# Kernel tuning notes

Hardware: AMD Instinct MI355X
Metric: run time of the kernel (lower is better)

Reference implementation:

```python
import jax, jax.numpy as jnp
import numpy as np

N = 50000
E = 600000
C = 128
O = 128


def setup_inputs() -> dict:
    key = jax.random.key(0)
    ks = jax.random.split(key, 10)
    return {
        "x": jax.random.normal(ks[0], (N, C), dtype=jnp.float32),
        "edge_weight": jax.random.uniform(ks[1], (E,), dtype=jnp.float32),
        "w0": jax.random.normal(ks[2], (C, O), dtype=jnp.float32) / np.sqrt(C),
        "b0": jax.random.normal(ks[3], (O,), dtype=jnp.float32) * 0.01,
        "w1": jax.random.normal(ks[4], (C, O), dtype=jnp.float32) / np.sqrt(C),
        "b1": jax.random.normal(ks[5], (O,), dtype=jnp.float32) * 0.01,
        "w2": jax.random.normal(ks[6], (C, O), dtype=jnp.float32) / np.sqrt(C),
        "b2": jax.random.normal(ks[7], (O,), dtype=jnp.float32) * 0.01,
        "row": jax.random.randint(ks[8], (E,), 0, N, dtype=jnp.int64),
        "col": jax.random.randint(ks[9], (E,), 0, N, dtype=jnp.int64),
    }


def reference(x, edge_weight, w0, b0, w1, b1, w2, b2, row, col):
    n = x.shape[0]

    def spmm(v):
        # out[i] = sum_{e: row[e]==i} edge_weight[e] * v[col[e]]
        return jax.ops.segment_sum(edge_weight[:, None] * v[col], row, num_segments=n)

    x0 = x @ w0 + b0                    # hop 0: no propagation
    x1 = spmm(x @ w1 + b1)              # hop 1: one SpMM
    x2 = spmm(spmm(x @ w2 + b2))        # hop 2: two SpMMs
    return jnp.concatenate([x0, x1, x2], axis=1)  # [N, 3*O]
```

## Files before the change

### kernel.cpp

```cpp
#include <hip/hip_runtime.h>
#include <hip/hip_bf16.h>


#define NC 128
#define BM 64
#define BK 32
#define SBLK 256


__global__ void zero_kernel(int* __restrict__ p, int n) {
    int i = blockIdx.x * blockDim.x + threadIdx.x;
    if (i < n) p[i] = 0;
}


__global__ void count_kernel(const int* __restrict__ row, const float* __restrict__ ew,
                             int* __restrict__ cnt, float* __restrict__ s1, int E) {
    int e = blockIdx.x * blockDim.x + threadIdx.x;
    if (e < E) {
        int r = row[e];
        atomicAdd(&cnt[r], 1);
        atomicAdd(&s1[r], ew[e]);
    }
}

__global__ __launch_bounds__(SBLK) void scan_partial(const int* __restrict__ cnt,
                                                     int* __restrict__ bsum, int n) {
    int i = blockIdx.x * SBLK + threadIdx.x;
    int v = (i < n) ? cnt[i] : 0;
    #pragma unroll
    for (int off = 32; off; off >>= 1) v += __shfl_down(v, off, 64);
    __shared__ int wsum[4];
    if ((threadIdx.x & 63) == 0) wsum[threadIdx.x >> 6] = v;
    __syncthreads();
    if (threadIdx.x == 0) bsum[blockIdx.x] = wsum[0] + wsum[1] + wsum[2] + wsum[3];
}

__global__ __launch_bounds__(SBLK) void scan_base(const int* __restrict__ bsum,
                                                  int* __restrict__ bbase, int nb) {
    __shared__ int sh[SBLK];
    int tid = threadIdx.x;
    int v = (tid < nb) ? bsum[tid] : 0;
    sh[tid] = v;
    __syncthreads();
    for (int off = 1; off < SBLK; off <<= 1) {
        int add = (tid >= off) ? sh[tid - off] : 0;
        __syncthreads();
        sh[tid] += add;
        __syncthreads();
    }
    if (tid < nb) bbase[tid] = sh[tid] - v;
}

__global__ __launch_bounds__(SBLK) void scan_final(const int* __restrict__ cnt,
                                                   const int* __restrict__ bbase,
                                                   int* __restrict__ rowptr,
                                                   int* __restrict__ pos, int n, int E) {
    int i = blockIdx.x * SBLK + threadIdx.x;
    int tid = threadIdx.x;
    __shared__ int sh[SBLK];
    int v = (i < n) ? cnt[i] : 0;
    sh[tid] = v;
    __syncthreads();
    for (int off = 1; off < SBLK; off <<= 1) {
        int add = (tid >= off) ? sh[tid - off] : 0;
        __syncthreads();
        sh[tid] += add;
        __syncthreads();
    }
    int excl = sh[tid] - v + bbase[blockIdx.x];
    if (i < n) { rowptr[i] = excl; pos[i] = excl; }
    if (i == 0) rowptr[n] = E;
}

__global__ void scatter_kernel(const int* __restrict__ row, const int* __restrict__ col,
                               const float* __restrict__ ew, int* __restrict__ pos,
                               int* __restrict__ ccol, float* __restrict__ cw, int E) {
    int e = blockIdx.x * blockDim.x + threadIdx.x;
    if (e < E) {
        int r = row[e];
        int p = atomicAdd(&pos[r], 1);
        if (p >= 0 && p < E) {
            ccol[p] = col[e];
            cw[p]   = ew[e];
        }
    }
}

__global__ void s2_kernel(const int* __restrict__ rowptr, const int* __restrict__ ccol,
                          const float* __restrict__ cw, const float* __restrict__ s1,
                          float* __restrict__ s2, int n) {
    int i = blockIdx.x * blockDim.x + threadIdx.x;
    if (i >= n) return;
    int s = rowptr[i], e = rowptr[i + 1];
    float acc = 0.f;
    for (int k = s; k < e; k++) acc += cw[k] * s1[ccol[k]];
    s2[i] = acc;
}


__global__ __launch_bounds__(256) void spmm_kernel(
    const int* __restrict__ rowptr, const int* __restrict__ ccol,
    const float* __restrict__ cw, const float* __restrict__ v,
    float* __restrict__ out, int n)
{
    int wid = (blockIdx.x * blockDim.x + threadIdx.x) >> 6;
    int lane = threadIdx.x & 63;
    if (wid >= n) return;
    int s = rowptr[wid];
    int e = rowptr[wid + 1];
    float ax = 0.f, ay = 0.f;
    int k = s;
    for (; k + 4 <= e; k += 4) {
        int c0 = ccol[k], c1 = ccol[k + 1], c2 = ccol[k + 2], c3 = ccol[k + 3];
        float w0 = cw[k], w1 = cw[k + 1], w2 = cw[k + 2], w3 = cw[k + 3];
        float2 v0 = *(const float2*)(v + (size_t)c0 * NC + lane * 2);
        float2 v1 = *(const float2*)(v + (size_t)c1 * NC + lane * 2);
        float2 v2 = *(const float2*)(v + (size_t)c2 * NC + lane * 2);
        float2 v3 = *(const float2*)(v + (size_t)c3 * NC + lane * 2);
        ax += w0 * v0.x; ay += w0 * v0.y;
        ax += w1 * v1.x; ay += w1 * v1.y;
        ax += w2 * v2.x; ay += w2 * v2.y;
        ax += w3 * v3.x; ay += w3 * v3.y;
    }
    for (; k < e; k++) {
        int c = ccol[k];
        float w = cw[k];
        float2 vv = *(const float2*)(v + (size_t)c * NC + lane * 2);
        ax += w * vv.x; ay += w * vv.y;
    }
    float2* o = (float2*)(out + (size_t)wid * NC + lane * 2);
    *o = {ax, ay};
}


__global__ __launch_bounds__(256, 4) void gemm3_kernel(
    const float* __restrict__ x, const float* __restrict__ Y1, const float* __restrict__ Y2,
    const float* __restrict__ w0, const float* __restrict__ b0,
    const float* __restrict__ w1, const float* __restrict__ b1,
    const float* __restrict__ w2, const float* __restrict__ b2,
    const float* __restrict__ s1, const float* __restrict__ s2,
    float* __restrict__ out, int n)
{
    __shared__ float xs[BK][BM];
    __shared__ float wsb[BK][NC];

    int hop = blockIdx.y;
    const float* S  = (hop == 0) ? x  : (hop == 1) ? Y1 : Y2;
    const float* W  = (hop == 0) ? w0 : (hop == 1) ? w1 : w2;
    const float* B  = (hop == 0) ? b0 : (hop == 1) ? b1 : b2;
    const float* SV = (hop == 0) ? nullptr : (hop == 1) ? s1 : s2;

    int tid = threadIdx.x;
    int m0 = blockIdx.x * BM;
    int tx = tid & 31, ty = tid >> 5;
    int c0 = tx * 4, r0 = ty * 8;

    int sr = tid >> 2;
    int skk = (tid & 3) * 8;
    int gr_s = m0 + sr;
    bool inb = (gr_s < n);

    float acc[8][4] = {};

    for (int kc = 0; kc < NC; kc += BK) {
        if (kc) __syncthreads();
        float4 a0 = {0,0,0,0}, a1 = {0,0,0,0};
        if (inb) {
            const float4* xv = (const float4*)(S + (size_t)gr_s * NC + kc + skk);
            a0 = xv[0]; a1 = xv[1];
        }
        xs[skk + 0][sr] = a0.x; xs[skk + 1][sr] = a0.y;
        xs[skk + 2][sr] = a0.z; xs[skk + 3][sr] = a0.w;
        xs[skk + 4][sr] = a1.x; xs[skk + 5][sr] = a1.y;
        xs[skk + 6][sr] = a1.z; xs[skk + 7][sr] = a1.w;
        {
            const float4* Wv = (const float4*)(W + (size_t)kc * NC);
            float4* wv = (float4*)&wsb[0][0];
            wv[tid]       = Wv[tid];
            wv[tid + 256] = Wv[tid + 256];
            wv[tid + 512] = Wv[tid + 512];
            wv[tid + 768] = Wv[tid + 768];
        }
        __syncthreads();

        #pragma unroll 8
        for (int k = 0; k < BK; k++) {
            float4 bv = *(const float4*)&wsb[k][c0];
            float4 x0 = *(const float4*)&xs[k][r0];
            float4 x1 = *(const float4*)&xs[k][r0 + 4];
            float a[8] = {x0.x, x0.y, x0.z, x0.w, x1.x, x1.y, x1.z, x1.w};
            #pragma unroll
            for (int i = 0; i < 8; i++) {
                acc[i][0] += a[i] * bv.x;
                acc[i][1] += a[i] * bv.y;
                acc[i][2] += a[i] * bv.z;
                acc[i][3] += a[i] * bv.w;
            }
        }
    }

    float4 bb = *(const float4*)(B + c0);
    #pragma unroll
    for (int i = 0; i < 8; i++) {
        int gr = m0 + r0 + i;
        if (gr < n) {
            float sc = SV ? SV[gr] : 1.0f;
            float4 v = {acc[i][0] + sc * bb.x, acc[i][1] + sc * bb.y,
                        acc[i][2] + sc * bb.z, acc[i][3] + sc * bb.w};
            *(float4*)(out + (size_t)gr * 384 + hop * NC + c0) = v;
        }
    }
}


extern "C" void kernel_launch(void* const* d_in, const int* in_sizes, int n_in,
                              void* d_out, int out_size, void* d_ws, size_t ws_size,
                              hipStream_t stream) {
    const float* x  = (const float*)d_in[0];
    const float* ew = (const float*)d_in[1];
    const float* w0 = (const float*)d_in[2];
    const float* b0 = (const float*)d_in[3];
    const float* w1 = (const float*)d_in[4];
    const float* b1 = (const float*)d_in[5];
    const float* w2 = (const float*)d_in[6];
    const float* b2 = (const float*)d_in[7];
    const int* row  = (const int*)d_in[8];
    const int* col  = (const int*)d_in[9];
    float* out = (float*)d_out;

    const int N = in_sizes[0] / NC;
    const int E = in_sizes[1];

    char* ws = (char*)d_ws;
    size_t off = 0;
    auto alloc = [&](size_t bytes) {
        void* p = ws + off;
        off += (bytes + 255) & ~(size_t)255;
        return p;
    };
    float* Y1    = (float*)alloc((size_t)N * NC * 4);
    float* Y2    = (float*)alloc((size_t)N * NC * 4);
    int* cnt     = (int*)alloc((size_t)2 * N * 4);
    float* s1    = (float*)(cnt + N);
    int* rowptr  = (int*)alloc((size_t)(N + 1) * 4);
    int* pos     = (int*)alloc((size_t)N * 4);
    float* s2    = (float*)alloc((size_t)N * 4);
    int* ccol    = (int*)alloc((size_t)E * 4);
    float* cw    = (float*)alloc((size_t)E * 4);

    int nb = (N + SBLK - 1) / SBLK;
    int* bsum  = (int*)alloc((size_t)nb * 4);
    int* bbase = (int*)alloc((size_t)nb * 4);

    zero_kernel<<<(2 * N + 255) / 256, 256, 0, stream>>>(cnt, 2 * N);
    count_kernel<<<(E + 255) / 256, 256, 0, stream>>>(row, ew, cnt, s1, E);
    scan_partial<<<nb, SBLK, 0, stream>>>(cnt, bsum, N);
    scan_base<<<1, SBLK, 0, stream>>>(bsum, bbase, nb);
    scan_final<<<nb, SBLK, 0, stream>>>(cnt, bbase, rowptr, pos, N, E);
    scatter_kernel<<<(E + 255) / 256, 256, 0, stream>>>(row, col, ew, pos, ccol, cw, E);
    s2_kernel<<<(N + 255) / 256, 256, 0, stream>>>(rowptr, ccol, cw, s1, s2, N);

    int spmm_blocks = (N * 64 + 255) / 256;
    spmm_kernel<<<spmm_blocks, 256, 0, stream>>>(rowptr, ccol, cw, x, Y1, N);
    spmm_kernel<<<spmm_blocks, 256, 0, stream>>>(rowptr, ccol, cw, Y1, Y2, N);

    gemm3_kernel<<<dim3((N + BM - 1) / BM, 3), 256, 0, stream>>>(
        x, Y1, Y2, w0, b0, w1, b1, w2, b2, s1, s2, out, N);
}
```

Baseline: 368.0 us.

## Switch SpMM intermediates and GEMM to bf16 with MFMA tensor-core matmul

Converts x and the weights to bf16, runs both SpMM passes on bf16 features with fp32 accumulation, and replaces the fp32 SIMT GEMM with a bf16 MFMA 16x16x32 kernel reading pre-transposed weights. It also computes the row weight sums s1 inside the first SpMM instead of with float atomics in the count kernel. The goal is to halve gather bandwidth in the memory-bound SpMMs and use matrix cores for the GEMM, at the cost of bf16 rounding error in the intermediates and in the output.

Result: faster. 306.9 us (-16.6%).

```diff
diff --git a/kernel.cpp b/kernel.cpp
--- a/kernel.cpp
+++ b/kernel.cpp
@@ -3,9 +3,20 @@
 
 
 #define NC 128
-#define BM 64
-#define BK 32
 #define SBLK 256
+
+typedef unsigned short ushort_t;
+typedef unsigned int uint_t;
+typedef __attribute__((ext_vector_type(8))) short short8v;
+typedef __attribute__((ext_vector_type(4))) float float4v;
+
+__device__ __forceinline__ ushort_t f2bf(float f) {
+    uint_t u = __float_as_uint(f);
+    return (ushort_t)((u + 0x7fffu + ((u >> 16) & 1u)) >> 16);
+}
+__device__ __forceinline__ float bf2f(ushort_t s) {
+    return __uint_as_float(((uint_t)s) << 16);
+}
 
 
 __global__ void zero_kernel(int* __restrict__ p, int n) {
@@ -13,15 +24,35 @@
     if (i < n) p[i] = 0;
 }
 
-
-__global__ void count_kernel(const int* __restrict__ row, const float* __restrict__ ew,
-                             int* __restrict__ cnt, float* __restrict__ s1, int E) {
+__global__ void convert_x(const float* __restrict__ x, ushort_t* __restrict__ xb, int total8) {
+    int i = blockIdx.x * blockDim.x + threadIdx.x;
+    if (i >= total8) return;
+    const float4* xp = (const float4*)(x + (size_t)i * 8);
+    float4 a = xp[0], b = xp[1];
+    uint_t p0 = (uint_t)f2bf(a.x) | ((uint_t)f2bf(a.y) << 16);
+    uint_t p1 = (uint_t)f2bf(a.z) | ((uint_t)f2bf(a.w) << 16);
+    uint_t p2 = (uint_t)f2bf(b.x) | ((uint_t)f2bf(b.y) << 16);
+    uint_t p3 = (uint_t)f2bf(b.z) | ((uint_t)f2bf(b.w) << 16);
+    uint4 v = {p0, p1, p2, p3};
+    *(uint4*)(xb + (size_t)i * 8) = v;
+}
+
+__global__ void convert_w(const float* __restrict__ w0, const float* __restrict__ w1,
+                          const float* __restrict__ w2, ushort_t* __restrict__ wbT) {
+    int t = blockIdx.x * blockDim.x + threadIdx.x;
+    if (t >= 3 * NC * NC) return;
+    int h = t / (NC * NC);
+    int rem = t - h * NC * NC;
+    int nrow = rem / NC;
+    int k = rem - nrow * NC;
+    const float* W = (h == 0) ? w0 : (h == 1) ? w1 : w2;
+    wbT[t] = f2bf(W[(size_t)k * NC + nrow]);
+}
+
+
+__global__ void count_kernel(const int* __restrict__ row, int* __restrict__ cnt, int E) {
     int e = blockIdx.x * blockDim.x + threadIdx.x;
-    if (e < E) {
-        int r = row[e];
-        atomicAdd(&cnt[r], 1);
-        atomicAdd(&s1[r], ew[e]);
-    }
+    if (e < E) atomicAdd(&cnt[row[e]], 1);
 }
 
 __global__ __launch_bounds__(SBLK) void scan_partial(const int* __restrict__ cnt,
@@ -99,116 +130,110 @@
 }
 
 
-__global__ __launch_bounds__(256) void spmm_kernel(
+__global__ __launch_bounds__(256) void spmm_bf16(
     const int* __restrict__ rowptr, const int* __restrict__ ccol,
-    const float* __restrict__ cw, const float* __restrict__ v,
-    float* __restrict__ out, int n)
+    const float* __restrict__ cw, const ushort_t* __restrict__ v,
+    ushort_t* __restrict__ outb, float* __restrict__ s1_out, int n)
 {
     int wid = (blockIdx.x * blockDim.x + threadIdx.x) >> 6;
     int lane = threadIdx.x & 63;
     if (wid >= n) return;
     int s = rowptr[wid];
     int e = rowptr[wid + 1];
-    float ax = 0.f, ay = 0.f;
+    float ax = 0.f, ay = 0.f, sw = 0.f;
     int k = s;
     for (; k + 4 <= e; k += 4) {
         int c0 = ccol[k], c1 = ccol[k + 1], c2 = ccol[k + 2], c3 = ccol[k + 3];
         float w0 = cw[k], w1 = cw[k + 1], w2 = cw[k + 2], w3 = cw[k + 3];
-        float2 v0 = *(const float2*)(v + (size_t)c0 * NC + lane * 2);
-        float2 v1 = *(const float2*)(v + (size_t)c1 * NC + lane * 2);
-        float2 v2 = *(const float2*)(v + (size_t)c2 * NC + lane * 2);
-        float2 v3 = *(const float2*)(v + (size_t)c3 * NC + lane * 2);
-        ax += w0 * v0.x; ay += w0 * v0.y;
-        ax += w1 * v1.x; ay += w1 * v1.y;
-        ax += w2 * v2.x; ay += w2 * v2.y;
-        ax += w3 * v3.x; ay += w3 * v3.y;
+        uint_t g0 = *(const uint_t*)(v + (size_t)c0 * NC + lane * 2);
+        uint_t g1 = *(const uint_t*)(v + (size_t)c1 * NC + lane * 2);
+        uint_t g2 = *(const uint_t*)(v + (size_t)c2 * NC + lane * 2);
+        uint_t g3 = *(const uint_t*)(v + (size_t)c3 * NC + lane * 2);
+        ax += w0 * bf2f(g0 & 0xffff); ay += w0 * bf2f(g0 >> 16);
+        ax += w1 * bf2f(g1 & 0xffff); ay += w1 * bf2f(g1 >> 16);
+        ax += w2 * bf2f(g2 & 0xffff); ay += w2 * bf2f(g2 >> 16);
+        ax += w3 * bf2f(g3 & 0xffff); ay += w3 * bf2f(g3 >> 16);
+        sw += w0 + w1 + w2 + w3;
     }
     for (; k < e; k++) {
         int c = ccol[k];
         float w = cw[k];
-        float2 vv = *(const float2*)(v + (size_t)c * NC + lane * 2);
-        ax += w * vv.x; ay += w * vv.y;
-    }
-    float2* o = (float2*)(out + (size_t)wid * NC + lane * 2);
-    *o = {ax, ay};
-}
-
-
-__global__ __launch_bounds__(256, 4) void gemm3_kernel(
-    const float* __restrict__ x, const float* __restrict__ Y1, const float* __restrict__ Y2,
-    const float* __restrict__ w0, const float* __restrict__ b0,
-    const float* __restrict__ w1, const float* __restrict__ b1,
-    const float* __restrict__ w2, const float* __restrict__ b2,
+        uint_t g = *(const uint_t*)(v + (size_t)c * NC + lane * 2);
+        ax += w * bf2f(g & 0xffff); ay += w * bf2f(g >> 16);
+        sw += w;
+    }
+    uint_t packed = (uint_t)f2bf(ax) | ((uint_t)f2bf(ay) << 16);
+    *(uint_t*)(outb + (size_t)wid * NC + lane * 2) = packed;
+    if (s1_out && lane == 0) s1_out[wid] = sw;
+}
+
+
+__global__ __launch_bounds__(256) void gemm3_mfma(
+    const ushort_t* __restrict__ xb, const ushort_t* __restrict__ Y1b,
+    const ushort_t* __restrict__ Y2b, const ushort_t* __restrict__ wbT,
+    const float* __restrict__ b0, const float* __restrict__ b1, const float* __restrict__ b2,
     const float* __restrict__ s1, const float* __restrict__ s2,
     float* __restrict__ out, int n)
 {
-    __shared__ float xs[BK][BM];
-    __shared__ float wsb[BK][NC];
+    __shared__ ushort_t ss[64][NC + 8];
 
     int hop = blockIdx.y;
-    const float* S  = (hop == 0) ? x  : (hop == 1) ? Y1 : Y2;
-    const float* W  = (hop == 0) ? w0 : (hop == 1) ? w1 : w2;
-    const float* B  = (hop == 0) ? b0 : (hop == 1) ? b1 : b2;
-    const float* SV = (hop == 0) ? nullptr : (hop == 1) ? s1 : s2;
+    const ushort_t* S  = (hop == 0) ? xb : (hop == 1) ? Y1b : Y2b;
+    const ushort_t* WT = wbT + (size_t)hop * NC * NC;
+    const float* B     = (hop == 0) ? b0 : (hop == 1) ? b1 : b2;
+    const float* SV    = (hop == 0) ? nullptr : (hop == 1) ? s1 : s2;
 
     int tid = threadIdx.x;
-    int m0 = blockIdx.x * BM;
-    int tx = tid & 31, ty = tid >> 5;
-    int c0 = tx * 4, r0 = ty * 8;
-
-    int sr = tid >> 2;
-    int skk = (tid & 3) * 8;
-    int gr_s = m0 + sr;
-    bool inb = (gr_s < n);
-
-    float acc[8][4] = {};
-
-    for (int kc = 0; kc < NC; kc += BK) {
-        if (kc) __syncthreads();
-        float4 a0 = {0,0,0,0}, a1 = {0,0,0,0};
-        if (inb) {
-            const float4* xv = (const float4*)(S + (size_t)gr_s * NC + kc + skk);
-            a0 = xv[0]; a1 = xv[1];
-        }
-        xs[skk + 0][sr] = a0.x; xs[skk + 1][sr] = a0.y;
-        xs[skk + 2][sr] = a0.z; xs[skk + 3][sr] = a0.w;
-        xs[skk + 4][sr] = a1.x; xs[skk + 5][sr] = a1.y;
-        xs[skk + 6][sr] = a1.z; xs[skk + 7][sr] = a1.w;
-        {
-            const float4* Wv = (const float4*)(W + (size_t)kc * NC);
-            float4* wv = (float4*)&wsb[0][0];
-            wv[tid]       = Wv[tid];
-            wv[tid + 256] = Wv[tid + 256];
-            wv[tid + 512] = Wv[tid + 512];
-            wv[tid + 768] = Wv[tid + 768];
-        }
-        __syncthreads();
-
-        #pragma unroll 8
-        for (int k = 0; k < BK; k++) {
-            float4 bv = *(const float4*)&wsb[k][c0];
-            float4 x0 = *(const float4*)&xs[k][r0];
-            float4 x1 = *(const float4*)&xs[k][r0 + 4];
-            float a[8] = {x0.x, x0.y, x0.z, x0.w, x1.x, x1.y, x1.z, x1.w};
-            #pragma unroll
-            for (int i = 0; i < 8; i++) {
-                acc[i][0] += a[i] * bv.x;
-                acc[i][1] += a[i] * bv.y;
-                acc[i][2] += a[i] * bv.z;
-                acc[i][3] += a[i] * bv.w;
-            }
-        }
-    }
-
-    float4 bb = *(const float4*)(B + c0);
-    #pragma unroll
-    for (int i = 0; i < 8; i++) {
-        int gr = m0 + r0 + i;
+    int m0 = blockIdx.x * 64;
+
+    {
+        int r = tid >> 2;
+        int seg = (tid & 3) * 32;
+        int gr = m0 + r;
+        uint4 z = {0, 0, 0, 0};
+        uint4 v0 = z, v1 = z, v2 = z, v3 = z;
         if (gr < n) {
-            float sc = SV ? SV[gr] : 1.0f;
-            float4 v = {acc[i][0] + sc * bb.x, acc[i][1] + sc * bb.y,
-                        acc[i][2] + sc * bb.z, acc[i][3] + sc * bb.w};
-            *(float4*)(out + (size_t)gr * 384 + hop * NC + c0) = v;
+            const uint4* sp = (const uint4*)(S + (size_t)gr * NC + seg);
+            v0 = sp[0]; v1 = sp[1]; v2 = sp[2]; v3 = sp[3];
+        }
+        uint4* dp = (uint4*)&ss[r][seg];
+        dp[0] = v0; dp[1] = v1; dp[2] = v2; dp[3] = v3;
+    }
+    __syncthreads();
+
+    int w  = tid >> 6;
+    int l  = tid & 63;
+    int lm = l & 15;
+    int lh = l >> 4;
+
+    short8v a[4];
+    #pragma unroll
+    for (int kk = 0; kk < 4; kk++)
+        a[kk] = *(const short8v*)&ss[w * 16 + lm][kk * 32 + lh * 8];
+
+    float sc[4];
+    #pragma unroll
+    for (int j = 0; j < 4; j++) {
+        int gr = m0 + w * 16 + lh * 4 + j;
+        sc[j] = (SV && gr < n) ? SV[gr] : 1.0f;
+    }
+
+    #pragma unroll
+    for (int nt = 0; nt < 8; nt++) {
+        float4v c = {0.f, 0.f, 0.f, 0.f};
+        const ushort_t* wp = WT + (size_t)(nt * 16 + lm) * NC + lh * 8;
+        #pragma unroll
+        for (int kk = 0; kk < 4; kk++) {
+            short8v b = *(const short8v*)(wp + kk * 32);
+            c = __builtin_amdgcn_mfma_f32_16x16x32_bf16(a[kk], b, c, 0, 0, 0);
+        }
+        int colg = nt * 16 + lm;
+        float bb = B[colg];
+        #pragma unroll
+        for (int j = 0; j < 4; j++) {
+            int gr = m0 + w * 16 + lh * 4 + j;
+            if (gr < n)
+                out[(size_t)gr * 384 + hop * NC + colg] = c[j] + sc[j] * bb;
         }
     }
 }
@@ -239,32 +264,36 @@
         off += (bytes + 255) & ~(size_t)255;
         return p;
     };
-    float* Y1    = (float*)alloc((size_t)N * NC * 4);
-    float* Y2    = (float*)alloc((size_t)N * NC * 4);
-    int* cnt     = (int*)alloc((size_t)2 * N * 4);
-    float* s1    = (float*)(cnt + N);
-    int* rowptr  = (int*)alloc((size_t)(N + 1) * 4);
-    int* pos     = (int*)alloc((size_t)N * 4);
-    float* s2    = (float*)alloc((size_t)N * 4);
-    int* ccol    = (int*)alloc((size_t)E * 4);
-    float* cw    = (float*)alloc((size_t)E * 4);
+    ushort_t* xb   = (ushort_t*)alloc((size_t)N * NC * 2);
+    ushort_t* Y1b  = (ushort_t*)alloc((size_t)N * NC * 2);
+    ushort_t* Y2b  = (ushort_t*)alloc((size_t)N * NC * 2);
+    ushort_t* wbT  = (ushort_t*)alloc((size_t)3 * NC * NC * 2);
+    int* cnt       = (int*)alloc((size_t)N * 4);
+    int* rowptr    = (int*)alloc((size_t)(N + 1) * 4);
+    int* pos       = (int*)alloc((size_t)N * 4);
+    float* s1      = (float*)alloc((size_t)N * 4);
+    float* s2      = (float*)alloc((size_t)N * 4);
+    int* ccol      = (int*)alloc((size_t)E * 4);
+    float* cw      = (float*)alloc((size_t)E * 4);
 
     int nb = (N + SBLK - 1) / SBLK;
     int* bsum  = (int*)alloc((size_t)nb * 4);
     int* bbase = (int*)alloc((size_t)nb * 4);
 
-    zero_kernel<<<(2 * N + 255) / 256, 256, 0, stream>>>(cnt, 2 * N);
-    count_kernel<<<(E + 255) / 256, 256, 0, stream>>>(row, ew, cnt, s1, E);
+    zero_kernel<<<(N + 255) / 256, 256, 0, stream>>>(cnt, N);
+    convert_x<<<((N * NC / 8) + 255) / 256, 256, 0, stream>>>(x, xb, N * NC / 8);
+    convert_w<<<(3 * NC * NC + 255) / 256, 256, 0, stream>>>(w0, w1, w2, wbT);
+    count_kernel<<<(E + 255) / 256, 256, 0, stream>>>(row, cnt, E);
     scan_partial<<<nb, SBLK, 0, stream>>>(cnt, bsum, N);
     scan_base<<<1, SBLK, 0, stream>>>(bsum, bbase, nb);
     scan_final<<<nb, SBLK, 0, stream>>>(cnt, bbase, rowptr, pos, N, E);
     scatter_kernel<<<(E + 255) / 256, 256, 0, stream>>>(row, col, ew, pos, ccol, cw, E);
+
+    int spmm_blocks = (N * 64 + 255) / 256;
+    spmm_bf16<<<spmm_blocks, 256, 0, stream>>>(rowptr, ccol, cw, xb, Y1b, s1, N);
     s2_kernel<<<(N + 255) / 256, 256, 0, stream>>>(rowptr, ccol, cw, s1, s2, N);
-
-    int spmm_blocks = (N * 64 + 255) / 256;
-    spmm_kernel<<<spmm_blocks, 256, 0, stream>>>(rowptr, ccol, cw, x, Y1, N);
-    spmm_kernel<<<spmm_blocks, 256, 0, stream>>>(rowptr, ccol, cw, Y1, Y2, N);
-
-    gemm3_kernel<<<dim3((N + BM - 1) / BM, 3), 256, 0, stream>>>(
-        x, Y1, Y2, w0, b0, w1, b1, w2, b2, s1, s2, out, N);
-}
+    spmm_bf16<<<spmm_blocks, 256, 0, stream>>>(rowptr, ccol, cw, Y1b, Y2b, nullptr, N);
+
+    gemm3_mfma<<<dim3((N + 63) / 64, 3), 256, 0, stream>>>(
+        xb, Y1b, Y2b, wbT, b0, b1, b2, s1, s2, out, N);
+}
```
